# Performance work log

Measured on AMD Instinct MI355X. Metric: run time of the kernel, lower is better.

## Reference

```python
import jax, jax.numpy as jnp
import numpy as np

B, T = 512, 64
C_IN, C_HID, C_OUT = 512, 512, 256
SIZE_INP = C_IN + C_HID + C_OUT  # 1280
SIZE_GATES = 4 * C_HID           # 2048


def setup_inputs() -> dict:
    key = jax.random.key(0)
    k1, k2, k3, k4, k5 = jax.random.split(key, 5)
    s_rnn = 1.0 / np.sqrt(SIZE_INP)
    s_feat = 1.0 / np.sqrt(C_HID)
    return {
        "z": jax.random.normal(k1, (B, T, C_IN, 1, 1), dtype=jnp.float32),
        "r0": jnp.zeros((B, C_OUT, 1, 1), dtype=jnp.float32),
        "h0": jnp.zeros((B, C_HID, 1, 1), dtype=jnp.float32),
        "c0": jnp.zeros((B, C_HID, 1, 1), dtype=jnp.float32),
        "W_rnn": jax.random.uniform(k2, (SIZE_GATES, SIZE_INP), jnp.float32, -s_rnn, s_rnn),
        "b_rnn": jax.random.uniform(k3, (SIZE_GATES,), jnp.float32, -s_rnn, s_rnn),
        "W_feat": jax.random.uniform(k4, (C_OUT, C_HID), jnp.float32, -s_feat, s_feat),
        "b_feat": jax.random.uniform(k5, (C_OUT,), jnp.float32, -s_feat, s_feat),
    }


def reference(z, r0, h0, c0, W_rnn, b_rnn, W_feat, b_feat):
    # 1x1 convs on [B,C,1,1] tensors are plain matmuls over channels.
    zs = z[..., 0, 0]  # [B, T, C_in]

    def step(carry, z_t):
        r, h, c = carry  # [B,Cout], [B,H], [B,H]
        inp = jnp.concatenate([r, h, z_t], axis=1)          # [B, 1280]
        gates = inp @ W_rnn.T + b_rnn                       # [B, 4H]
        f, i, s, o = jnp.split(gates, 4, axis=1)            # torch.chunk order
        c_n = jax.nn.sigmoid(f) * c + jax.nn.sigmoid(i) * jnp.tanh(s)
        h_n = jax.nn.sigmoid(o) * jnp.tanh(c_n)
        r_n = r + h_n @ W_feat.T + b_feat
        return (r_n, h_n, c_n), None

    carry0 = (r0[..., 0, 0], h0[..., 0, 0], c0[..., 0, 0])
    (r, h, c), _ = jax.lax.scan(step, carry0, jnp.swapaxes(zs, 0, 1))
    return r[..., None, None], (h[..., None, None], c[..., None, None])
```

## Files before the change

### kernel.cpp

```cpp
#include <hip/hip_runtime.h>
#include <hip/hip_fp16.h>


using f32x4 = __attribute__((ext_vector_type(4))) float;
using f16x8 = __attribute__((ext_vector_type(8))) _Float16;
using fp16x2 = __attribute__((ext_vector_type(2))) __fp16;

union U4H8 { uint4 u; f16x8 h; fp16x2 p[4]; };

__device__ __forceinline__ float sigm(float x){ return 1.0f/(1.0f + __expf(-x)); }
__device__ __forceinline__ float tanhfast(float x){
  x = fminf(fmaxf(x, -30.f), 30.f);
  float e = __expf(2.0f*x);
  return (e - 1.0f)/(e + 1.0f);
}

#define MFMA16(a,b,c) __builtin_amdgcn_mfma_f32_16x16x32_f16((a).h,(b).h,(c),0,0,0)


__global__ void k_wft(const float* __restrict__ wf, float* __restrict__ wft){
  int idx = blockIdx.x*256 + threadIdx.x;
  int c = idx & 511; int j = idx >> 9;
  wft[c*256 + j] = wf[idx];
}

__global__ void k_bias2(const float* __restrict__ wrnn, const float* __restrict__ brnn,
                        const float* __restrict__ bfeat, float* __restrict__ biasp){
  int wv = (blockIdx.x*256 + threadIdx.x) >> 6;
  int lane = threadIdx.x & 63;
  int g = (wv&3)*512 + (wv>>2);
  const float* wr = wrnn + (size_t)g*1280;
  float s = 0.f;
  for (int j = lane; j < 256; j += 64) s += bfeat[j]*wr[j];
  for (int off = 32; off; off >>= 1) s += __shfl_down(s, off, 64);
  if (lane == 0) biasp[wv] = brnn[g] + s;
}

__global__ void k_whp4(const float* __restrict__ wrnn, const float* __restrict__ wft,
                       float* __restrict__ whp_part){
  int s = blockIdx.x >> 8;
  int tl = blockIdx.x & 255;
  int bn = tl & 31, bk = tl >> 5;
  __shared__ float wrs[64][37];
  __shared__ float wfs[64][37];
  int tid = threadIdx.x;
  int tn = tid & 15, tk = tid >> 4;
  float accv[4][4];
  #pragma unroll
  for (int x=0;x<4;x++) for (int y=0;y<4;y++) accv[x][y]=0.f;
  for (int jc = s*64; jc < s*64+64; jc += 32){
    __syncthreads();
    for (int idx = tid; idx < 64*32; idx += 256){
      int r = idx >> 5, j = idx & 31;
      int n = bn*64 + r; int g = (n&3)*512 + (n>>2);
      wrs[r][j] = wrnn[(size_t)g*1280 + jc + j];
      wfs[r][j] = wft[(bk*64 + r)*256 + jc + j];
    }
    __syncthreads();
    for (int j=0;j<32;j++){
      float a[4], b[4];
      #pragma unroll
      for (int x=0;x<4;x++){ a[x] = wfs[tk*4+x][j]; b[x] = wrs[tn*4+x][j]; }
      #pragma unroll
      for (int x=0;x<4;x++)
        #pragma unroll
        for (int y=0;y<4;y++) accv[x][y] += a[x]*b[y];
    }
  }
  float* dst = whp_part + (size_t)s*1048576;
  for (int x=0;x<4;x++){
    int kk = bk*64 + tk*4 + x;
    for (int y=0;y<4;y++){
      int n = bn*64 + tn*4 + y;
      dst[(size_t)kk*2048 + n] = accv[x][y];
    }
  }
}

__global__ void k_whpadd(const float* __restrict__ p, float* __restrict__ o){
  int i = (blockIdx.x*256 + threadIdx.x)*4;
  float4 a = *(const float4*)(p + i);
  float4 b = *(const float4*)(p + 1048576 + i);
  float4 c = *(const float4*)(p + 2097152 + i);
  float4 d = *(const float4*)(p + 3145728 + i);
  float4 r;
  r.x = a.x+b.x+c.x+d.x; r.y = a.y+b.y+c.y+d.y;
  r.z = a.z+b.z+c.z+d.z; r.w = a.w+b.w+c.w+d.w;
  *(float4*)(o + i) = r;
}

__global__ void k_rinit(const float* __restrict__ r0, const float* __restrict__ h0,
                        const float* __restrict__ wft, const float* __restrict__ bfeat,
                        float* __restrict__ rd32, __half* __restrict__ rd16){
  __shared__ float hs[512];
  int row = blockIdx.x; int j = threadIdx.x;
  for (int k = threadIdx.x; k < 512; k += 256) hs[k] = h0[row*512 + k];
  __syncthreads();
  float acc = 0.f;
  for (int k=0;k<512;k++) acc += hs[k]*wft[k*256 + j];
  float rr = r0[row*256 + j] - acc - bfeat[j];
  rd32[row*256 + j] = rr;
  int ridx = (((row>>4)*8 + (j>>5))*64 + (row&15) + (((j&31)>>3)<<4))*8 + (j&7);
  rd16[ridx] = __float2half(rr);
}

__global__ void k_packh0(const float* __restrict__ h0, const float* __restrict__ c0,
                         __half* __restrict__ h16, float* __restrict__ c32){
  int idx = blockIdx.x*256 + threadIdx.x;
  int e = idx & 7, l = (idx>>3) & 63, kc = (idx>>9) & 15, mt = idx >> 13;
  int row = mt*16 + (l&15);
  int k = kc*32 + ((l>>4)<<3) + e;
  h16[idx] = __float2half(h0[row*512 + k]);
  c32[idx] = c0[idx];
}

__global__ void k_pack(const float* __restrict__ wrnn, const float* __restrict__ whp32,
                       const float* __restrict__ wfeat, __half* __restrict__ dst,
                       int mode, int NT16, int KCH){
  int tot = NT16*KCH*512;
  for (int idx = blockIdx.x*256 + threadIdx.x; idx < tot; idx += gridDim.x*256){
    int e = idx & 7; int l = (idx>>3) & 63;
    int kc = (idx>>9) % KCH; int nt = (idx>>9) / KCH;
    int k = kc*32 + ((l>>4)<<3) + e;
    int n = nt*16 + (l&15);
    float v;
    if (mode == 0){
      int g = (n&3)*512 + (n>>2);
      if (k < 256) v = wrnn[(size_t)g*1280 + k];
      else         v = whp32[(size_t)(k-256)*2048 + n] + wrnn[(size_t)g*1280 + k];
    } else if (mode == 2){
      int g = (n&3)*512 + (n>>2);
      v = wrnn[(size_t)g*1280 + 768 + k];
    } else {
      v = wfeat[(size_t)n*512 + k];
    }
    dst[idx] = __float2half(v);
  }
}

__global__ void k_zpackall(const float* __restrict__ z, __half* __restrict__ z16){
  int u = blockIdx.x*256 + threadIdx.x;
  int k0 = (u & 63) * 8;
  int b4 = (u >> 6) & 127;
  int t  = u >> 13;
  int b = b4 * 4;
  int frag = (t*32 + (b>>4))*16 + (k0>>5);
  uint4 wv[4];
  #pragma unroll
  for (int j=0;j<4;j++){
    const float4* src = (const float4*)(z + ((size_t)((b+j)*64 + t))*512 + k0);
    float4 f0 = src[0], f1 = src[1];
    U4H8 a;
    a.p[0] = __builtin_amdgcn_cvt_pkrtz(f0.x, f0.y);
    a.p[1] = __builtin_amdgcn_cvt_pkrtz(f0.z, f0.w);
    a.p[2] = __builtin_amdgcn_cvt_pkrtz(f1.x, f1.y);
    a.p[3] = __builtin_amdgcn_cvt_pkrtz(f1.z, f1.w);
    wv[j] = a.u;
  }
  uint4* dst = (uint4*)z16 + (size_t)frag*64 + (b & 15) + (((k0 & 31) >> 3) << 4);
  #pragma unroll
  for (int j=0;j<4;j++) dst[j] = wv[j];
}

__global__ __launch_bounds__(512) void k_gzbig(const __half* __restrict__ z16,
    const __half* __restrict__ bpz, const float* __restrict__ biasp,
    __half* __restrict__ gz){
  const int tid = threadIdx.x, lane = tid & 63, w = tid >> 6;
  const int wr = w >> 2, wc = w & 3;
  const int xcd = blockIdx.x & 7;
  const int bn  = (blockIdx.x >> 3) & 15;
  const int bmh = blockIdx.x >> 7;
  const int bm  = xcd*32 + bmh;
  const int tt = bm >> 2, bq = bm & 3;
  const int mt0 = tt*32 + bq*8 + wr*4;
  const int nt0 = bn*8 + wc*2;
  const uint4* A = (const uint4*)z16 + (size_t)(mt0*16)*64 + lane;
  const uint4* B = (const uint4*)bpz + (size_t)(nt0*16)*64 + lane;
  f32x4 acc[4][2];
  #pragma unroll
  for (int mi=0;mi<4;mi++){ acc[mi][0]=(f32x4){0,0,0,0}; acc[mi][1]=(f32x4){0,0,0,0}; }
  #pragma unroll 2
  for (int kc=0; kc<16; ++kc){
    U4H8 b0v, b1v;
    b0v.u = B[kc*64];
    b1v.u = B[(16+kc)*64];
    #pragma unroll
    for (int mi=0; mi<4; mi++){
      U4H8 a;
      a.u = A[(mi*16 + kc)*64];
      acc[mi][0] = MFMA16(a, b0v, acc[mi][0]);
      acc[mi][1] = MFMA16(a, b1v, acc[mi][1]);
    }
  }
  #pragma unroll
  for (int ns=0; ns<2; ns++){
    int n = (nt0 + ns)*16 + (lane & 15);
    float bp = biasp[n];
    #pragma unroll
    for (int mi=0; mi<4; mi++){
      #pragma unroll
      for (int i=0; i<4; i++){
        int brow = bq*128 + wr*64 + mi*16 + ((lane>>4)<<2) + i;
        gz[((size_t)(tt*512 + brow))*2048 + n] = __float2half(acc[mi][ns][i] + bp);
      }
    }
  }
}

__global__ __launch_bounds__(576) void k_stepF(
    const __half* __restrict__ rd16_in, const __half* __restrict__ h16_in,
    float* __restrict__ rd32,
    __half* __restrict__ rd16_out, __half* __restrict__ h16_out,
    float* __restrict__ c32,
    const __half* __restrict__ gz,
    const __half* __restrict__ bp_rec, const __half* __restrict__ bf_pack,
    const float* __restrict__ bfeat,
    float* __restrict__ out_h, float* __restrict__ out_c, float* __restrict__ out_r,
    int step, int mode){
  __shared__ float cls[64][69];
  const int tid = threadIdx.x, lane = tid & 63;
  const int bid = blockIdx.x;
  const int bm = (bid>>3) & 7;
  const int bn = (bid&7)*4 + (bid>>6);

  if (mode == 0 && tid < 512){
    const int w = tid >> 6, wr = w >> 2, wc = w & 3;
    f32x4 a0A=(f32x4){0,0,0,0}, a0B=(f32x4){0,0,0,0};
    f32x4 a1A=(f32x4){0,0,0,0}, a1B=(f32x4){0,0,0,0};
    const int mtA = bm*4 + wr*2;
    const int nt  = bn*4 + wc;
    const uint4* a0p = (const uint4*)rd16_in + (size_t)(mtA*8)*64 + lane;
    const uint4* a1p = a0p + 8*64;
    const uint4* h0p = (const uint4*)h16_in + (size_t)(mtA*16)*64 + lane;
    const uint4* h1p = h0p + 16*64;
    const uint4* bp  = (const uint4*)bp_rec + (size_t)(nt*24)*64 + lane;
    #pragma unroll
    for (int kc=0; kc<4; ++kc){
      U4H8 a0,a1,b;
      a0.u = a0p[kc*64]; a1.u = a1p[kc*64]; b.u = bp[kc*64];
      a0A = MFMA16(a0,b,a0A);
      a1A = MFMA16(a1,b,a1A);
    }
    #pragma unroll
    for (int kc=4; kc<8; ++kc){
      U4H8 a0,a1,b;
      a0.u = a0p[kc*64]; a1.u = a1p[kc*64]; b.u = bp[kc*64];
      a0B = MFMA16(a0,b,a0B);
      a1B = MFMA16(a1,b,a1B);
    }
    #pragma unroll 4
    for (int kc=0; kc<8; ++kc){
      U4H8 a0,a1,b;
      a0.u = h0p[kc*64]; a1.u = h1p[kc*64]; b.u = bp[(8+kc)*64];
      a0A = MFMA16(a0,b,a0A);
      a1A = MFMA16(a1,b,a1A);
    }
    #pragma unroll 4
    for (int kc=8; kc<16; ++kc){
      U4H8 a0,a1,b;
      a0.u = h0p[kc*64]; a1.u = h1p[kc*64]; b.u = bp[(8+kc)*64];
      a0B = MFMA16(a0,b,a0B);
      a1B = MFMA16(a1,b,a1B);
    }
    const f32x4 acc0 = a0A + a0B;
    const f32x4 acc1 = a1A + a1B;
    #pragma unroll
    for (int i=0; i<4; i++){
      cls[wr*32 +      ((lane>>4)<<2) + i][wc*16 + (lane&15)] = acc0[i];
      cls[wr*32 + 16 + ((lane>>4)<<2) + i][wc*16 + (lane&15)] = acc1[i];
    }
  } else if (tid >= 512){
    const int mt = (bid>>3) & 31;
    const int nc = bid & 7;
    f32x4 racc0 = (f32x4){0,0,0,0}, racc1 = (f32x4){0,0,0,0};
    const uint4* hp  = (const uint4*)h16_in + (size_t)(mt*16)*64 + lane;
    const uint4* bf0 = (const uint4*)bf_pack + (size_t)((nc*2)*16)*64 + lane;
    const uint4* bf1 = bf0 + 16*64;
    #pragma unroll 4
    for (int kc=0; kc<16; ++kc){
      U4H8 a,b0,b1;
      a.u = hp[kc*64]; b0.u = bf0[kc*64]; b1.u = bf1[kc*64];
      racc0 = MFMA16(a,b0,racc0);
      racc1 = MFMA16(a,b1,racc1);
    }
    #pragma unroll
    for (int ns=0; ns<2; ns++){
      const f32x4 rv = ns ? racc1 : racc0;
      const int col = (nc*2+ns)*16 + (lane&15);
      const float bfv = bfeat[col];
      #pragma unroll
      for (int i=0;i<4;i++){
        const int grow = mt*16 + ((lane>>4)<<2) + i;
        const size_t x = (size_t)grow*256 + col;
        const float rr = rv[i] + rd32[x] + bfv;
        if (mode == 1){
          out_r[x] = rr;
        } else {
          rd32[x] = rr;
          const int ridx = (((grow>>4)*8 + (col>>5))*64
                            + (grow&15) + (((col&31)>>3)<<4))*8 + (col&7);
          rd16_out[ridx] = __float2half(rr);
        }
      }
    }
  }

  if (mode == 0){
    __syncthreads();
    if (tid < 512){
      const __half* gzt = gz + (size_t)step*1048576;
      #pragma unroll
      for (int rep=0; rep<2; rep++){
        int idx = rep*512 + tid;
        int jl = idx & 15, row = idx >> 4;
        int grow = bm*64 + row;
        int j = bn*16 + jl;
        const __half2* gp = (const __half2*)(gzt + (size_t)grow*2048 + bn*64 + jl*4);
        __half2 p0 = gp[0], p1 = gp[1];
        float g0 = cls[row][jl*4+0] + __half2float(p0.x);
        float g1 = cls[row][jl*4+1] + __half2float(p0.y);
        float g2 = cls[row][jl*4+2] + __half2float(p1.x);
        float g3 = cls[row][jl*4+3] + __half2float(p1.y);
        float cold = c32[(size_t)grow*512 + j];
        float f  = sigm(g0);
        float ii = sigm(g1);
        float s  = tanhfast(g2);
        float o  = sigm(g3);
        float cn = f*cold + ii*s;
        float hn = o*tanhfast(cn);
        c32[(size_t)grow*512 + j] = cn;
        int hidx = (((grow>>4)*16 + (j>>5))*64 + (grow&15) + (((j&31)>>3)<<4))*8 + (j&7);
        h16_out[hidx] = __float2half(hn);
        if (step == 63){
          out_h[(size_t)grow*512 + j] = hn;
          out_c[(size_t)grow*512 + j] = cn;
        }
      }
    }
  }
}

extern "C" void kernel_launch(void* const* d_in, const int* in_sizes, int n_in,
                              void* d_out, int out_size, void* d_ws, size_t ws_size,
                              hipStream_t stream){
  const float* z     = (const float*)d_in[0];
  const float* r0    = (const float*)d_in[1];
  const float* h0    = (const float*)d_in[2];
  const float* c0    = (const float*)d_in[3];
  const float* wrnn  = (const float*)d_in[4];
  const float* brnn  = (const float*)d_in[5];
  const float* wfeat = (const float*)d_in[6];
  const float* bfeat = (const float*)d_in[7];
  float* out = (float*)d_out;

  char* wsb = (char*)d_ws;
  size_t off = 0;
  auto alloc = [&](size_t bytes)->char*{
    char* p = wsb + off; off = (off + bytes + 255) & ~(size_t)255; return p;
  };
  __half* z16     = (__half*)alloc((size_t)64*512*512*2);
  __half* bp_rec  = (__half*)alloc((size_t)128*24*512*2);
  __half* bpz     = (__half*)alloc((size_t)128*16*512*2);
  __half* bf_pack = (__half*)alloc((size_t)16*16*512*2);
  float*  biasp   = (float*) alloc(2048*4);
  float*  wft32   = (float*) alloc((size_t)512*256*4);
  __half* h16A    = (__half*)alloc((size_t)512*512*2);
  __half* h16B    = (__half*)alloc((size_t)512*512*2);
  __half* rd16A   = (__half*)alloc((size_t)512*256*2);
  __half* rd16B   = (__half*)alloc((size_t)512*256*2);
  float*  rd32    = (float*) alloc((size_t)512*256*4);
  float*  c32     = (float*) alloc((size_t)512*512*4);
  __half* gz      = (__half*)alloc((size_t)64*512*2048*2);
  (void)ws_size;
  float* whp32    = (float*)gz;
  float* whp_part = (float*)gz + 1048576;

  k_wft     <<<dim3(512),  dim3(256), 0, stream>>>(wfeat, wft32);
  k_bias2   <<<dim3(512),  dim3(256), 0, stream>>>(wrnn, brnn, bfeat, biasp);
  k_whp4    <<<dim3(1024), dim3(256), 0, stream>>>(wrnn, wft32, whp_part);
  k_whpadd  <<<dim3(1024), dim3(256), 0, stream>>>(whp_part, whp32);
  k_rinit   <<<dim3(512),  dim3(256), 0, stream>>>(r0, h0, wft32, bfeat, rd32, rd16A);
  k_packh0  <<<dim3(1024), dim3(256), 0, stream>>>(h0, c0, h16A, c32);
  k_pack    <<<dim3(1024), dim3(256), 0, stream>>>(wrnn, whp32, wfeat, bp_rec, 0, 128, 24);
  k_pack    <<<dim3(1024), dim3(256), 0, stream>>>(wrnn, whp32, wfeat, bpz,    2, 128, 16);
  k_pack    <<<dim3(64),   dim3(256), 0, stream>>>(wrnn, whp32, wfeat, bf_pack,3,  16, 16);
  k_zpackall<<<dim3(2048), dim3(256), 0, stream>>>(z, z16);
  k_gzbig   <<<dim3(4096), dim3(512), 0, stream>>>(z16, bpz, biasp, gz);

  __half* h16in = h16A;  __half* h16out = h16B;
  __half* rd16in = rd16A; __half* rd16out = rd16B;
  for (int t = 1; t <= 64; ++t){
    k_stepF<<<dim3(256), dim3(576), 0, stream>>>(
        rd16in, h16in, rd32, rd16out, h16out, c32, gz,
        bp_rec, bf_pack, bfeat,
        out + 131072, out + 393216, (float*)nullptr, t-1, 0);
    __half* th;
    th = h16in; h16in = h16out; h16out = th;
    th = rd16in; rd16in = rd16out; rd16out = th;
  }
  k_stepF<<<dim3(256), dim3(576), 0, stream>>>(
      rd16in, h16in, rd32, rd16out, h16out, c32, gz,
      bp_rec, bf_pack, bfeat,
      (float*)nullptr, (float*)nullptr, out, 64, 1);
}
```

Measured before the change: 813.8 us.

## Halve per-block tile in recurrent step kernel and double the grid to 512 blocks

Each step block now computes a 32-row by 64-gate tile instead of 64 rows, with one MFMA chain per wave instead of two, and the feature-projection warp handles a single 16-column tile. The grid doubles to 512 blocks so all 256 CUs get work and each block's critical path is shorter, which targets the latency-bound per-step kernel. The cost is that B-weight fragments are reloaded by twice as many blocks, and each wave has less instruction-level parallelism.

```diff
diff --git a/kernel.cpp b/kernel.cpp
--- a/kernel.cpp
+++ b/kernel.cpp
@@ -217,90 +217,81 @@
     const float* __restrict__ bfeat,
     float* __restrict__ out_h, float* __restrict__ out_c, float* __restrict__ out_r,
     int step, int mode){
-  __shared__ float cls[64][69];
+  __shared__ float cls[32][69];
   const int tid = threadIdx.x, lane = tid & 63;
   const int bid = blockIdx.x;
-  const int bm = (bid>>3) & 7;
-  const int bn = (bid&7)*4 + (bid>>6);
+  const int bm = bid >> 5;
+  const int bn = (bid & 7)*4 + ((bid >> 3) & 3);
 
   if (mode == 0 && tid < 512){
     const int w = tid >> 6, wr = w >> 2, wc = w & 3;
-    f32x4 a0A=(f32x4){0,0,0,0}, a0B=(f32x4){0,0,0,0};
-    f32x4 a1A=(f32x4){0,0,0,0}, a1B=(f32x4){0,0,0,0};
-    const int mtA = bm*4 + wr*2;
+    const int mtA = bm*2 + wr;
     const int nt  = bn*4 + wc;
-    const uint4* a0p = (const uint4*)rd16_in + (size_t)(mtA*8)*64 + lane;
-    const uint4* a1p = a0p + 8*64;
-    const uint4* h0p = (const uint4*)h16_in + (size_t)(mtA*16)*64 + lane;
-    const uint4* h1p = h0p + 16*64;
-    const uint4* bp  = (const uint4*)bp_rec + (size_t)(nt*24)*64 + lane;
+    const uint4* ap = (const uint4*)rd16_in + (size_t)(mtA*8)*64 + lane;
+    const uint4* hp = (const uint4*)h16_in + (size_t)(mtA*16)*64 + lane;
+    const uint4* bp = (const uint4*)bp_rec + (size_t)(nt*24)*64 + lane;
+    f32x4 aA = (f32x4){0,0,0,0}, aB = (f32x4){0,0,0,0};
     #pragma unroll
     for (int kc=0; kc<4; ++kc){
-      U4H8 a0,a1,b;
-      a0.u = a0p[kc*64]; a1.u = a1p[kc*64]; b.u = bp[kc*64];
-      a0A = MFMA16(a0,b,a0A);
-      a1A = MFMA16(a1,b,a1A);
+      U4H8 a,b;
+      a.u = ap[kc*64]; b.u = bp[kc*64];
+      aA = MFMA16(a,b,aA);
     }
     #pragma unroll
     for (int kc=4; kc<8; ++kc){
-      U4H8 a0,a1,b;
-      a0.u = a0p[kc*64]; a1.u = a1p[kc*64]; b.u = bp[kc*64];
-      a0B = MFMA16(a0,b,a0B);
-      a1B = MFMA16(a1,b,a1B);
+      U4H8 a,b;
+      a.u = ap[kc*64]; b.u = bp[kc*64];
+      aB = MFMA16(a,b,aB);
     }
     #pragma unroll 4
     for (int kc=0; kc<8; ++kc){
-      U4H8 a0,a1,b;
-      a0.u = h0p[kc*64]; a1.u = h1p[kc*64]; b.u = bp[(8+kc)*64];
-      a0A = MFMA16(a0,b,a0A);
-      a1A = MFMA16(a1,b,a1A);
+      U4H8 a,b;
+      a.u = hp[kc*64]; b.u = bp[(8+kc)*64];
+      aA = MFMA16(a,b,aA);
     }
     #pragma unroll 4
     for (int kc=8; kc<16; ++kc){
-      U4H8 a0,a1,b;
-      a0.u = h0p[kc*64]; a1.u = h1p[kc*64]; b.u = bp[(8+kc)*64];
-      a0B = MFMA16(a0,b,a0B);
-      a1B = MFMA16(a1,b,a1B);
-    }
-    const f32x4 acc0 = a0A + a0B;
-    const f32x4 acc1 = a1A + a1B;
-    #pragma unroll
-    for (int i=0; i<4; i++){
-      cls[wr*32 +      ((lane>>4)<<2) + i][wc*16 + (lane&15)] = acc0[i];
-      cls[wr*32 + 16 + ((lane>>4)<<2) + i][wc*16 + (lane&15)] = acc1[i];
-    }
+      U4H8 a,b;
+      a.u = hp[kc*64]; b.u = bp[(8+kc)*64];
+      aB = MFMA16(a,b,aB);
+    }
+    const f32x4 acc = aA + aB;
+    #pragma unroll
+    for (int i=0; i<4; i++)
+      cls[wr*16 + ((lane>>4)<<2) + i][wc*16 + (lane&15)] = acc[i];
   } else if (tid >= 512){
-    const int mt = (bid>>3) & 31;
-    const int nc = bid & 7;
-    f32x4 racc0 = (f32x4){0,0,0,0}, racc1 = (f32x4){0,0,0,0};
-    const uint4* hp  = (const uint4*)h16_in + (size_t)(mt*16)*64 + lane;
-    const uint4* bf0 = (const uint4*)bf_pack + (size_t)((nc*2)*16)*64 + lane;
-    const uint4* bf1 = bf0 + 16*64;
+    const int mt = bid >> 4;
+    const int nc = bid & 15;
+    const uint4* hp = (const uint4*)h16_in + (size_t)(mt*16)*64 + lane;
+    const uint4* bf = (const uint4*)bf_pack + (size_t)(nc*16)*64 + lane;
+    f32x4 r0v = (f32x4){0,0,0,0}, r1v = (f32x4){0,0,0,0};
     #pragma unroll 4
-    for (int kc=0; kc<16; ++kc){
-      U4H8 a,b0,b1;
-      a.u = hp[kc*64]; b0.u = bf0[kc*64]; b1.u = bf1[kc*64];
-      racc0 = MFMA16(a,b0,racc0);
-      racc1 = MFMA16(a,b1,racc1);
-    }
-    #pragma unroll
-    for (int ns=0; ns<2; ns++){
-      const f32x4 rv = ns ? racc1 : racc0;
-      const int col = (nc*2+ns)*16 + (lane&15);
-      const float bfv = bfeat[col];
-      #pragma unroll
-      for (int i=0;i<4;i++){
-        const int grow = mt*16 + ((lane>>4)<<2) + i;
-        const size_t x = (size_t)grow*256 + col;
-        const float rr = rv[i] + rd32[x] + bfv;
-        if (mode == 1){
-          out_r[x] = rr;
-        } else {
-          rd32[x] = rr;
-          const int ridx = (((grow>>4)*8 + (col>>5))*64
-                            + (grow&15) + (((col&31)>>3)<<4))*8 + (col&7);
-          rd16_out[ridx] = __float2half(rr);
-        }
+    for (int kc=0; kc<8; ++kc){
+      U4H8 a,b;
+      a.u = hp[kc*64]; b.u = bf[kc*64];
+      r0v = MFMA16(a,b,r0v);
+    }
+    #pragma unroll 4
+    for (int kc=8; kc<16; ++kc){
+      U4H8 a,b;
+      a.u = hp[kc*64]; b.u = bf[kc*64];
+      r1v = MFMA16(a,b,r1v);
+    }
+    const f32x4 racc = r0v + r1v;
+    const int col = nc*16 + (lane&15);
+    const float bfv = bfeat[col];
+    #pragma unroll
+    for (int i=0;i<4;i++){
+      const int grow = mt*16 + ((lane>>4)<<2) + i;
+      const size_t x = (size_t)grow*256 + col;
+      const float rr = racc[i] + rd32[x] + bfv;
+      if (mode == 1){
+        out_r[x] = rr;
+      } else {
+        rd32[x] = rr;
+        const int ridx = (((grow>>4)*8 + (col>>5))*64
+                          + (grow&15) + (((col&31)>>3)<<4))*8 + (col&7);
+        rd16_out[ridx] = __float2half(rr);
       }
     }
   }
@@ -308,33 +299,29 @@
   if (mode == 0){
     __syncthreads();
     if (tid < 512){
+      const int jl = tid & 15, row = tid >> 4;
+      const int grow = bm*32 + row;
+      const int j = bn*16 + jl;
       const __half* gzt = gz + (size_t)step*1048576;
-      #pragma unroll
-      for (int rep=0; rep<2; rep++){
-        int idx = rep*512 + tid;
-        int jl = idx & 15, row = idx >> 4;
-        int grow = bm*64 + row;
-        int j = bn*16 + jl;
-        const __half2* gp = (const __half2*)(gzt + (size_t)grow*2048 + bn*64 + jl*4);
-        __half2 p0 = gp[0], p1 = gp[1];
-        float g0 = cls[row][jl*4+0] + __half2float(p0.x);
-        float g1 = cls[row][jl*4+1] + __half2float(p0.y);
-        float g2 = cls[row][jl*4+2] + __half2float(p1.x);
-        float g3 = cls[row][jl*4+3] + __half2float(p1.y);
-        float cold = c32[(size_t)grow*512 + j];
-        float f  = sigm(g0);
-        float ii = sigm(g1);
-        float s  = tanhfast(g2);
-        float o  = sigm(g3);
-        float cn = f*cold + ii*s;
-        float hn = o*tanhfast(cn);
-        c32[(size_t)grow*512 + j] = cn;
-        int hidx = (((grow>>4)*16 + (j>>5))*64 + (grow&15) + (((j&31)>>3)<<4))*8 + (j&7);
-        h16_out[hidx] = __float2half(hn);
-        if (step == 63){
-          out_h[(size_t)grow*512 + j] = hn;
-          out_c[(size_t)grow*512 + j] = cn;
-        }
+      const __half2* gp = (const __half2*)(gzt + (size_t)grow*2048 + bn*64 + jl*4);
+      __half2 p0 = gp[0], p1 = gp[1];
+      float g0 = cls[row][jl*4+0] + __half2float(p0.x);
+      float g1 = cls[row][jl*4+1] + __half2float(p0.y);
+      float g2 = cls[row][jl*4+2] + __half2float(p1.x);
+      float g3 = cls[row][jl*4+3] + __half2float(p1.y);
+      float cold = c32[(size_t)grow*512 + j];
+      float f  = sigm(g0);
+      float ii = sigm(g1);
+      float s  = tanhfast(g2);
+      float o  = sigm(g3);
+      float cn = f*cold + ii*s;
+      float hn = o*tanhfast(cn);
+      c32[(size_t)grow*512 + j] = cn;
+      int hidx = (((grow>>4)*16 + (j>>5))*64 + (grow&15) + (((j&31)>>3)<<4))*8 + (j&7);
+      h16_out[hidx] = __float2half(hn);
+      if (step == 63){
+        out_h[(size_t)grow*512 + j] = hn;
+        out_c[(size_t)grow*512 + j] = cn;
       }
     }
   }
@@ -390,7 +377,7 @@
   __half* h16in = h16A;  __half* h16out = h16B;
   __half* rd16in = rd16A; __half* rd16out = rd16B;
   for (int t = 1; t <= 64; ++t){
-    k_stepF<<<dim3(256), dim3(576), 0, stream>>>(
+    k_stepF<<<dim3(512), dim3(576), 0, stream>>>(
         rd16in, h16in, rd32, rd16out, h16out, c32, gz,
         bp_rec, bf_pack, bfeat,
         out + 131072, out + 393216, (float*)nullptr, t-1, 0);
@@ -398,7 +385,7 @@
     th = h16in; h16in = h16out; h16out = th;
     th = rd16in; rd16in = rd16out; rd16out = th;
   }
-  k_stepF<<<dim3(256), dim3(576), 0, stream>>>(
+  k_stepF<<<dim3(512), dim3(576), 0, stream>>>(
       rd16in, h16in, rd32, rd16out, h16out, c32, gz,
       bp_rec, bf_pack, bfeat,
       (float*)nullptr, (float*)nullptr, out, 64, 1);
```

Result: slower. 923.4 us (+13.5%).
